# Kernel optimization log

Measured on AMD Instinct MI355X. Metric: run time of the kernel, lower is better.

The kernel has to match this reference:

```python
import jax, jax.numpy as jnp
import numpy as np

K_IN = 9      # input_patch_size
K_OUT = 3     # output_patch_size
C_IN = 4      # nb_of_input_features
C_OUT = 2     # nb_of_output_features
HID = 50      # int_layer_width
B, H, W = 16, 128, 128
CUT = K_IN // 2 - K_OUT // 2  # border pixels cut from output (3)


def _unfold(x, k):
    # x: [B, C, H, W] -> [B, C*k*k, L] with torch unfold ordering (c, ki, kj)
    b, c, h, w = x.shape
    ho, wo = h - k + 1, w - k + 1
    cols = jnp.stack([x[:, :, i:i + ho, j:j + wo]
                      for i in range(k) for j in range(k)], axis=2)  # [B,C,k*k,ho,wo]
    return cols.reshape(b, c * k * k, ho * wo)


def _fold_add(patches, oh, ow):
    # patches: [B, C, k, k, ho, wo] -> overlap-add into [B, C, oh, ow]
    b, c, k, _, ho, wo = patches.shape
    out = jnp.zeros((b, c, oh, ow), dtype=patches.dtype)
    for i in range(k):
        for j in range(k):
            out = out.at[:, :, i:i + ho, j:j + wo].add(patches[:, :, i, j])
    return out


def setup_inputs() -> dict:
    key = jax.random.key(0)
    ks = jax.random.split(key, 7)
    f_in = C_IN * K_IN * K_IN      # 324
    f_out = C_OUT * K_OUT * K_OUT  # 18
    s1 = 1.0 / np.sqrt(f_in)
    s2 = 1.0 / np.sqrt(HID)
    return {
        "x": jax.random.normal(ks[0], (B, C_IN, H, W), dtype=jnp.float32),
        "W1": jax.random.uniform(ks[1], (f_in, HID), jnp.float32, -s1, s1),
        "b1": jax.random.uniform(ks[2], (HID,), jnp.float32, -s1, s1),
        "W2": jax.random.uniform(ks[3], (HID, HID), jnp.float32, -s2, s2),
        "b2": jax.random.uniform(ks[4], (HID,), jnp.float32, -s2, s2),
        "W3": jax.random.uniform(ks[5], (HID, f_out), jnp.float32, -s2, s2),
        "b3": jax.random.uniform(ks[6], (f_out,), jnp.float32, -s2, s2),
    }


def reference(x, W1, b1, W2, b2, W3, b3):
    b, c, h, w = x.shape
    oh, ow = h - 2 * CUT, w - 2 * CUT          # 122, 122
    ho, wo = h - K_IN + 1, w - K_IN + 1        # 120, 120 (= oh-K_OUT+1)
    # unfold -> [B, L, C_in*K_in^2] -> flatten rows
    cols = _unfold(x, K_IN)                    # [B, 324, L]
    feats = cols.transpose(0, 2, 1).reshape(b * ho * wo, -1)
    # 3-layer MLP
    hmid = jax.nn.relu(feats @ W1 + b1)
    hmid = jax.nn.relu(hmid @ W2 + b2)
    out = hmid @ W3 + b3                       # [B*L, C_out*K_out^2]
    # fold (overlap-add), torch feature ordering (c, ki, kj)
    patches = out.reshape(b, ho, wo, C_OUT, K_OUT, K_OUT)
    patches = patches.transpose(0, 3, 4, 5, 1, 2)  # [B, C_out, k, k, ho, wo]
    res = _fold_add(patches, oh, ow)
    # divisor = fold(unfold(ones)) -> per-pixel overlap count
    ones_patches = jnp.ones((1, 1, K_OUT, K_OUT, ho, wo), dtype=x.dtype)
    divisor = _fold_add(ones_patches, oh, ow)  # [1,1,oh,ow]
    return res / divisor
```

## Files before the change

kernel.cpp:

```cpp
#include <hip/hip_runtime.h>
#include <hip/hip_bf16.h>

#define BATCH   16
#define C_INF   4
#define H_IN    128
#define W_IN    128
#define HID     50
#define F_OUT   18
#define HO      120
#define WO      120
#define OH      122
#define OW      122
#define NPOS    (BATCH * HO * WO)
#define MBLK    128
#define NBLKS   (NPOS / MBLK)

#define NB1     (11*4*2*64*8)
#define NB2     (2*4*2*64*8)
#define NB3     (2*2*2*64*8)
#define NWF     (NB1 + NB2 + NB3)
#define NXP     (BATCH*C_INF*H_IN*W_IN)
#define WOFF    (NPOS * F_OUT)

typedef float  v4f    __attribute__((ext_vector_type(4)));
typedef short  short8 __attribute__((ext_vector_type(8)));
typedef __bf16 v8bf   __attribute__((ext_vector_type(8)));
typedef int    v4i    __attribute__((ext_vector_type(4)));
typedef uint   u32x4  __attribute__((ext_vector_type(4)));
typedef u32x4  u32x4_a4 __attribute__((aligned(4)));

__device__ inline short f2bf_hi(float x) {
    __hip_bfloat16 h = __float2bfloat16(x);
    return __builtin_bit_cast(short, h);
}
__device__ inline float bf2f(short s) {
    __hip_bfloat16 h = __builtin_bit_cast(__hip_bfloat16, s);
    return __bfloat162float(h);
}
__device__ inline uint hipair(uint a, uint b) { return __builtin_amdgcn_perm(b, a, 0x07060302u); }
__device__ inline uint lopair(uint a, uint b) { return __builtin_amdgcn_perm(b, a, 0x05040100u); }

__device__ inline int slot_to_k1(int s, int qb, int e) {
    if (s < 9) {
        int pair = s*4 + qb;
        int c = pair/9, ki = pair - c*9;
        return c*81 + ki*9 + e;
    }
    int r = (s-9)*32 + qb*8 + e;
    if (r >= 36) return -1;
    int c = r/9, ki = r - c*9;
    return c*81 + ki*9 + 8;
}

__global__ __launch_bounds__(256)
void prep_kernel(const float* __restrict__ x,
                 const float* __restrict__ W1, const float* __restrict__ W2,
                 const float* __restrict__ W3,
                 uint* __restrict__ xp, short* __restrict__ wf)
{
    int i = blockIdx.x * 256 + threadIdx.x;
    if (i < NXP) {
        float v = x[i];
        short hi = f2bf_hi(v);
        short lo = f2bf_hi(v - bf2f(hi));
        xp[i] = ((uint)(ushort)hi << 16) | (uint)(ushort)lo;
        return;
    }
    i -= NXP;
    if (i >= NWF) return;
    float val;
    int p;
    if (i < NB1) {
        int t = i;
        int e = t & 7, lane = (t >> 3) & 63; p = (t >> 9) & 1;
        int rest = t >> 10;
        int u = rest & 3, s = rest >> 2;
        int k = slot_to_k1(s, lane >> 4, e);
        int n = u*16 + (lane & 15);
        val = (k >= 0 && n < HID) ? W1[k*HID + n] : 0.f;
    } else if (i < NB1 + NB2) {
        int t = i - NB1;
        int e = t & 7, lane = (t >> 3) & 63; p = (t >> 9) & 1;
        int rest = t >> 10;
        int u = rest & 3, s = rest >> 2;
        int k = s*32 + ((lane >> 4) << 3) + e;
        int n = u*16 + (lane & 15);
        val = (k < HID && n < HID) ? W2[k*HID + n] : 0.f;
    } else {
        int t = i - NB1 - NB2;
        int e = t & 7, lane = (t >> 3) & 63; p = (t >> 9) & 1;
        int rest = t >> 10;
        int u = rest & 1, s = rest >> 1;
        int k = s*32 + ((lane >> 4) << 3) + e;
        int n = u*16 + (lane & 15);
        val = (k < HID && n < F_OUT) ? W3[k*F_OUT + n] : 0.f;
    }
    short hi = f2bf_hi(val);
    wf[i] = (p == 0) ? hi : f2bf_hi(val - bf2f(hi));
}

__global__ __launch_bounds__(256, 4)
void mfma_mlp(const uint* __restrict__ xp,
              const float* __restrict__ b1, const float* __restrict__ b2,
              const float* __restrict__ b3,
              const short* __restrict__ wf, float* __restrict__ out3)
{
    __shared__ short h_hi[128 * 72];
    __shared__ short h_lo[128 * 72];

    const int tid  = threadIdx.x;
    const int lane = tid & 63;
    const int w    = tid >> 6;
    const int wm   = w >> 1, wn = w & 1;
    const int q    = lane >> 4, col = lane & 15;
    const int mbase = blockIdx.x * MBLK;

    int xbase[4];
    #pragma unroll
    for (int t = 0; t < 4; ++t) {
        int pos = mbase + wm*64 + t*16 + col;
        int b   = pos / (HO*WO); int rem = pos - b*(HO*WO);
        int y   = rem / WO;      int xc  = rem - y*WO;
        xbase[t] = b*(C_INF*H_IN*W_IN) + y*W_IN + xc;
    }

    const v4i* B1 = (const v4i*)wf;
    const v4i* B2 = (const v4i*)(wf + NB1);
    const v4i* B3 = (const v4i*)(wf + NB1 + NB2);

    v4f acc[4][2];
    #pragma unroll
    for (int t = 0; t < 4; ++t)
        #pragma unroll
        for (int u = 0; u < 2; ++u)
            acc[t][u] = (v4f){0.f, 0.f, 0.f, 0.f};

    #pragma unroll 3
    for (int s = 0; s < 9; ++s) {
        const int pair = s*4 + q;
        const int c = pair/9, ki = pair - c*9;
        const int off = c*(H_IN*W_IN) + ki*W_IN;

        v4i bhv[2], blv[2];
        #pragma unroll
        for (int uu = 0; uu < 2; ++uu) {
            int u  = 2*wn + uu;
            int fb = ((s*4 + u)*2)*64 + lane;
            bhv[uu] = B1[fb];
            blv[uu] = B1[fb + 64];
        }

        u32x4 wa[4], wb[4];
        #pragma unroll
        for (int t = 0; t < 4; ++t) {
            const uint* p = &xp[xbase[t] + off];
            wa[t] = *(const u32x4_a4*)(p);
            wb[t] = *(const u32x4_a4*)(p + 4);
        }
        short8 ah[4], al[4];
        #pragma unroll
        for (int t = 0; t < 4; ++t) {
            u32x4 hh, ll;
            hh.x = hipair(wa[t].x, wa[t].y); hh.y = hipair(wa[t].z, wa[t].w);
            hh.z = hipair(wb[t].x, wb[t].y); hh.w = hipair(wb[t].z, wb[t].w);
            ll.x = lopair(wa[t].x, wa[t].y); ll.y = lopair(wa[t].z, wa[t].w);
            ll.z = lopair(wb[t].x, wb[t].y); ll.w = lopair(wb[t].z, wb[t].w);
            ah[t] = __builtin_bit_cast(short8, hh);
            al[t] = __builtin_bit_cast(short8, ll);
        }
        #pragma unroll
        for (int uu = 0; uu < 2; ++uu) {
            v8bf bh = __builtin_bit_cast(v8bf, bhv[uu]);
            v8bf bl = __builtin_bit_cast(v8bf, blv[uu]);
            #pragma unroll
            for (int t = 0; t < 4; ++t) {
                v8bf a_h = __builtin_bit_cast(v8bf, ah[t]);
                v8bf a_l = __builtin_bit_cast(v8bf, al[t]);
                acc[t][uu] = __builtin_amdgcn_mfma_f32_16x16x32_bf16(a_h, bh, acc[t][uu], 0, 0, 0);
                acc[t][uu] = __builtin_amdgcn_mfma_f32_16x16x32_bf16(a_l, bh, acc[t][uu], 0, 0, 0);
                acc[t][uu] = __builtin_amdgcn_mfma_f32_16x16x32_bf16(a_h, bl, acc[t][uu], 0, 0, 0);
            }
        }
    }
    #pragma unroll
    for (int sr = 0; sr < 2; ++sr) {
        const int s = 9 + sr;
        short8 ah[4], al[4];
        #pragma unroll
        for (int e = 0; e < 8; ++e) {
            int r = sr*32 + q*8 + e;
            bool valid = (r < 36);
            int c = valid ? r/9 : 0;
            int ki = r - c*9;
            int off = c*(H_IN*W_IN) + ki*W_IN + 8;
            #pragma unroll
            for (int t = 0; t < 4; ++t) {
                uint wv = valid ? xp[xbase[t] + off] : 0u;
                ah[t][e] = (short)(wv >> 16);
                al[t][e] = (short)(wv & 0xffffu);
            }
        }
        #pragma unroll
        for (int uu = 0; uu < 2; ++uu) {
            int u  = 2*wn + uu;
            int fb = ((s*4 + u)*2)*64 + lane;
            v8bf bh = __builtin_bit_cast(v8bf, B1[fb]);
            v8bf bl = __builtin_bit_cast(v8bf, B1[fb + 64]);
            #pragma unroll
            for (int t = 0; t < 4; ++t) {
                v8bf a_h = __builtin_bit_cast(v8bf, ah[t]);
                v8bf a_l = __builtin_bit_cast(v8bf, al[t]);
                acc[t][uu] = __builtin_amdgcn_mfma_f32_16x16x32_bf16(a_h, bh, acc[t][uu], 0, 0, 0);
                acc[t][uu] = __builtin_amdgcn_mfma_f32_16x16x32_bf16(a_l, bh, acc[t][uu], 0, 0, 0);
                acc[t][uu] = __builtin_amdgcn_mfma_f32_16x16x32_bf16(a_h, bl, acc[t][uu], 0, 0, 0);
            }
        }
    }

    #pragma unroll
    for (int uu = 0; uu < 2; ++uu) {
        int j = (2*wn + uu)*16 + col;
        float bias = (j < HID) ? b1[j] : 0.f;
        #pragma unroll
        for (int t = 0; t < 4; ++t) {
            #pragma unroll
            for (int r = 0; r < 4; ++r) {
                float v = fmaxf(acc[t][uu][r] + bias, 0.f);
                int m = wm*64 + t*16 + q*4 + r;
                short hi = f2bf_hi(v);
                h_hi[m*72 + j] = hi;
                h_lo[m*72 + j] = f2bf_hi(v - bf2f(hi));
            }
        }
    }
    __syncthreads();

    v4f acc2[4][2];
    #pragma unroll
    for (int t = 0; t < 4; ++t)
        #pragma unroll
        for (int u = 0; u < 2; ++u)
            acc2[t][u] = (v4f){0.f, 0.f, 0.f, 0.f};

    #pragma unroll
    for (int s = 0; s < 2; ++s) {
        short8 ah2[4], al2[4];
        #pragma unroll
        for (int t = 0; t < 4; ++t) {
            int m = wm*64 + t*16 + col;
            ah2[t] = *(const short8*)&h_hi[m*72 + s*32 + q*8];
            al2[t] = *(const short8*)&h_lo[m*72 + s*32 + q*8];
        }
        #pragma unroll
        for (int uu = 0; uu < 2; ++uu) {
            int u  = 2*wn + uu;
            int fb = ((s*4 + u)*2)*64 + lane;
            v8bf bh = __builtin_bit_cast(v8bf, B2[fb]);
            v8bf bl = __builtin_bit_cast(v8bf, B2[fb + 64]);
            #pragma unroll
            for (int t = 0; t < 4; ++t) {
                v8bf a_h = __builtin_bit_cast(v8bf, ah2[t]);
                v8bf a_l = __builtin_bit_cast(v8bf, al2[t]);
                acc2[t][uu] = __builtin_amdgcn_mfma_f32_16x16x32_bf16(a_h, bh, acc2[t][uu], 0, 0, 0);
                acc2[t][uu] = __builtin_amdgcn_mfma_f32_16x16x32_bf16(a_l, bh, acc2[t][uu], 0, 0, 0);
                acc2[t][uu] = __builtin_amdgcn_mfma_f32_16x16x32_bf16(a_h, bl, acc2[t][uu], 0, 0, 0);
            }
        }
    }
    __syncthreads();

    #pragma unroll
    for (int uu = 0; uu < 2; ++uu) {
        int j = (2*wn + uu)*16 + col;
        float bias = (j < HID) ? b2[j] : 0.f;
        #pragma unroll
        for (int t = 0; t < 4; ++t) {
            #pragma unroll
            for (int r = 0; r < 4; ++r) {
                float v = fmaxf(acc2[t][uu][r] + bias, 0.f);
                int m = wm*64 + t*16 + q*4 + r;
                short hi = f2bf_hi(v);
                h_hi[m*72 + j] = hi;
                h_lo[m*72 + j] = f2bf_hi(v - bf2f(hi));
            }
        }
    }
    __syncthreads();

    v4f acc3[4];
    #pragma unroll
    for (int t = 0; t < 4; ++t) acc3[t] = (v4f){0.f, 0.f, 0.f, 0.f};

    #pragma unroll
    for (int s = 0; s < 2; ++s) {
        short8 ah3[4], al3[4];
        #pragma unroll
        for (int t = 0; t < 4; ++t) {
            int m = wm*64 + t*16 + col;
            ah3[t] = *(const short8*)&h_hi[m*72 + s*32 + q*8];
            al3[t] = *(const short8*)&h_lo[m*72 + s*32 + q*8];
        }
        int fb = ((s*2 + wn)*2)*64 + lane;
        v8bf bh = __builtin_bit_cast(v8bf, B3[fb]);
        v8bf bl = __builtin_bit_cast(v8bf, B3[fb + 64]);
        #pragma unroll
        for (int t = 0; t < 4; ++t) {
            v8bf a_h = __builtin_bit_cast(v8bf, ah3[t]);
            v8bf a_l = __builtin_bit_cast(v8bf, al3[t]);
            acc3[t] = __builtin_amdgcn_mfma_f32_16x16x32_bf16(a_h, bh, acc3[t], 0, 0, 0);
            acc3[t] = __builtin_amdgcn_mfma_f32_16x16x32_bf16(a_l, bh, acc3[t], 0, 0, 0);
            acc3[t] = __builtin_amdgcn_mfma_f32_16x16x32_bf16(a_h, bl, acc3[t], 0, 0, 0);
        }
    }
    __syncthreads();

    float* ot = (float*)h_hi;
    {
        int j = wn*16 + col;
        if (j < F_OUT) {
            float bias = b3[j];
            #pragma unroll
            for (int t = 0; t < 4; ++t) {
                #pragma unroll
                for (int r = 0; r < 4; ++r) {
                    int m = wm*64 + t*16 + q*4 + r;
                    ot[j*129 + m] = acc3[t][r] + bias;
                }
            }
        }
    }
    __syncthreads();
    for (int i = tid; i < F_OUT * 128; i += 256) {
        int j2 = i >> 7, m2 = i & 127;
        out3[j2*NPOS + mbase + m2] = ot[j2*129 + m2];
    }
}

__global__ __launch_bounds__(256)
void fold_kernel(const float* __restrict__ out3, float* __restrict__ out)
{
    const int idx = blockIdx.x * 256 + threadIdx.x;
    const int total = BATCH * 2 * OH * OW;
    if (idx >= total) return;

    int t = idx;
    const int ox = t % OW; t /= OW;
    const int oy = t % OH; t /= OH;
    const int c  = t & 1;  t >>= 1;
    const int b  = t;

    const int ylo = max(0, oy - 2), yhi = min(HO - 1, oy);
    const int xlo = max(0, ox - 2), xhi = min(WO - 1, ox);

    float s = 0.f;
    for (int y = ylo; y <= yhi; ++y) {
        const int ki = oy - y;
        for (int xx = xlo; xx <= xhi; ++xx) {
            const int kj = ox - xx;
            const int o  = (c*3 + ki)*3 + kj;
            s += out3[o*NPOS + (b*HO + y)*WO + xx];
        }
    }
    const float div = (float)((yhi - ylo + 1) * (xhi - xlo + 1));
    out[idx] = s / div;
}

extern "C" void kernel_launch(void* const* d_in, const int* in_sizes, int n_in,
                              void* d_out, int out_size, void* d_ws, size_t ws_size,
                              hipStream_t stream)
{
    const float* x  = (const float*)d_in[0];
    const float* W1 = (const float*)d_in[1];
    const float* b1 = (const float*)d_in[2];
    const float* W2 = (const float*)d_in[3];
    const float* b2 = (const float*)d_in[4];
    const float* W3 = (const float*)d_in[5];
    const float* b3 = (const float*)d_in[6];

    float* out3 = (float*)d_ws;
    short* wf   = (short*)d_ws + 2*(size_t)WOFF;
    uint*  xp   = (uint*)((char*)d_ws + (size_t)WOFF*4 + (size_t)NWF*2);

    const int nprep = (NXP + NWF + 255) / 256;
    prep_kernel<<<nprep, 256, 0, stream>>>(x, W1, W2, W3, xp, wf);

    mfma_mlp<<<NBLKS, 256, 0, stream>>>(xp, b1, b2, b3, wf, out3);

    const int total = BATCH * 2 * OH * OW;
    fold_kernel<<<(total + 255) / 256, 256, 0, stream>>>(out3, (float*)d_out);
}
```

Before: 124.7 us.

## Give each wave full hidden width and drop low-part split for layers 2-3

Each wave now owns 32 rows and all N columns, so the hidden activations it writes to shared memory are read back only by the same wave. That lets every __syncthreads be removed. Layers 2 and 3 drop the bf16 low-part activation term, cutting their MFMA count and shared-memory traffic. The output is stored straight to global as float4 instead of being staged through LDS. In exchange, each wave loads four B fragments per step instead of two, and layers 2-3 lose some accuracy from the bf16 hidden activations.

Measured after the change: 121.3 us. -2.7%, faster.

```diff
diff --git a/kernel.cpp b/kernel.cpp
--- a/kernel.cpp
+++ b/kernel.cpp
@@ -106,19 +106,18 @@
               const short* __restrict__ wf, float* __restrict__ out3)
 {
     __shared__ short h_hi[128 * 72];
-    __shared__ short h_lo[128 * 72];
 
     const int tid  = threadIdx.x;
     const int lane = tid & 63;
     const int w    = tid >> 6;
-    const int wm   = w >> 1, wn = w & 1;
     const int q    = lane >> 4, col = lane & 15;
     const int mbase = blockIdx.x * MBLK;
-
-    int xbase[4];
-    #pragma unroll
-    for (int t = 0; t < 4; ++t) {
-        int pos = mbase + wm*64 + t*16 + col;
+    const int mw    = w * 32;
+
+    int xbase[2];
+    #pragma unroll
+    for (int t = 0; t < 2; ++t) {
+        int pos = mbase + mw + t*16 + col;
         int b   = pos / (HO*WO); int rem = pos - b*(HO*WO);
         int y   = rem / WO;      int xc  = rem - y*WO;
         xbase[t] = b*(C_INF*H_IN*W_IN) + y*W_IN + xc;
@@ -128,11 +127,11 @@
     const v4i* B2 = (const v4i*)(wf + NB1);
     const v4i* B3 = (const v4i*)(wf + NB1 + NB2);
 
-    v4f acc[4][2];
-    #pragma unroll
-    for (int t = 0; t < 4; ++t)
-        #pragma unroll
-        for (int u = 0; u < 2; ++u)
+    v4f acc[2][4];
+    #pragma unroll
+    for (int t = 0; t < 2; ++t)
+        #pragma unroll
+        for (int u = 0; u < 4; ++u)
             acc[t][u] = (v4f){0.f, 0.f, 0.f, 0.f};
 
     #pragma unroll 3
@@ -141,25 +140,24 @@
         const int c = pair/9, ki = pair - c*9;
         const int off = c*(H_IN*W_IN) + ki*W_IN;
 
-        v4i bhv[2], blv[2];
-        #pragma unroll
-        for (int uu = 0; uu < 2; ++uu) {
-            int u  = 2*wn + uu;
+        v4i bhv[4], blv[4];
+        #pragma unroll
+        for (int u = 0; u < 4; ++u) {
             int fb = ((s*4 + u)*2)*64 + lane;
-            bhv[uu] = B1[fb];
-            blv[uu] = B1[fb + 64];
-        }
-
-        u32x4 wa[4], wb[4];
-        #pragma unroll
-        for (int t = 0; t < 4; ++t) {
+            bhv[u] = B1[fb];
+            blv[u] = B1[fb + 64];
+        }
+
+        u32x4 wa[2], wb[2];
+        #pragma unroll
+        for (int t = 0; t < 2; ++t) {
             const uint* p = &xp[xbase[t] + off];
             wa[t] = *(const u32x4_a4*)(p);
             wb[t] = *(const u32x4_a4*)(p + 4);
         }
-        short8 ah[4], al[4];
-        #pragma unroll
-        for (int t = 0; t < 4; ++t) {
+        short8 ah[2], al[2];
+        #pragma unroll
+        for (int t = 0; t < 2; ++t) {
             u32x4 hh, ll;
             hh.x = hipair(wa[t].x, wa[t].y); hh.y = hipair(wa[t].z, wa[t].w);
             hh.z = hipair(wb[t].x, wb[t].y); hh.w = hipair(wb[t].z, wb[t].w);
@@ -169,23 +167,23 @@
             al[t] = __builtin_bit_cast(short8, ll);
         }
         #pragma unroll
-        for (int uu = 0; uu < 2; ++uu) {
-            v8bf bh = __builtin_bit_cast(v8bf, bhv[uu]);
-            v8bf bl = __builtin_bit_cast(v8bf, blv[uu]);
-            #pragma unroll
-            for (int t = 0; t < 4; ++t) {
+        for (int u = 0; u < 4; ++u) {
+            v8bf bh = __builtin_bit_cast(v8bf, bhv[u]);
+            v8bf bl = __builtin_bit_cast(v8bf, blv[u]);
+            #pragma unroll
+            for (int t = 0; t < 2; ++t) {
                 v8bf a_h = __builtin_bit_cast(v8bf, ah[t]);
                 v8bf a_l = __builtin_bit_cast(v8bf, al[t]);
-                acc[t][uu] = __builtin_amdgcn_mfma_f32_16x16x32_bf16(a_h, bh, acc[t][uu], 0, 0, 0);
-                acc[t][uu] = __builtin_amdgcn_mfma_f32_16x16x32_bf16(a_l, bh, acc[t][uu], 0, 0, 0);
-                acc[t][uu] = __builtin_amdgcn_mfma_f32_16x16x32_bf16(a_h, bl, acc[t][uu], 0, 0, 0);
+                acc[t][u] = __builtin_amdgcn_mfma_f32_16x16x32_bf16(a_h, bh, acc[t][u], 0, 0, 0);
+                acc[t][u] = __builtin_amdgcn_mfma_f32_16x16x32_bf16(a_l, bh, acc[t][u], 0, 0, 0);
+                acc[t][u] = __builtin_amdgcn_mfma_f32_16x16x32_bf16(a_h, bl, acc[t][u], 0, 0, 0);
             }
         }
     }
     #pragma unroll
     for (int sr = 0; sr < 2; ++sr) {
         const int s = 9 + sr;
-        short8 ah[4], al[4];
+        short8 ah[2], al[2];
         #pragma unroll
         for (int e = 0; e < 8; ++e) {
             int r = sr*32 + q*8 + e;
@@ -194,145 +192,129 @@
             int ki = r - c*9;
             int off = c*(H_IN*W_IN) + ki*W_IN + 8;
             #pragma unroll
-            for (int t = 0; t < 4; ++t) {
+            for (int t = 0; t < 2; ++t) {
                 uint wv = valid ? xp[xbase[t] + off] : 0u;
                 ah[t][e] = (short)(wv >> 16);
                 al[t][e] = (short)(wv & 0xffffu);
             }
         }
         #pragma unroll
-        for (int uu = 0; uu < 2; ++uu) {
-            int u  = 2*wn + uu;
+        for (int u = 0; u < 4; ++u) {
             int fb = ((s*4 + u)*2)*64 + lane;
             v8bf bh = __builtin_bit_cast(v8bf, B1[fb]);
             v8bf bl = __builtin_bit_cast(v8bf, B1[fb + 64]);
             #pragma unroll
-            for (int t = 0; t < 4; ++t) {
+            for (int t = 0; t < 2; ++t) {
                 v8bf a_h = __builtin_bit_cast(v8bf, ah[t]);
                 v8bf a_l = __builtin_bit_cast(v8bf, al[t]);
-                acc[t][uu] = __builtin_amdgcn_mfma_f32_16x16x32_bf16(a_h, bh, acc[t][uu], 0, 0, 0);
-                acc[t][uu] = __builtin_amdgcn_mfma_f32_16x16x32_bf16(a_l, bh, acc[t][uu], 0, 0, 0);
-                acc[t][uu] = __builtin_amdgcn_mfma_f32_16x16x32_bf16(a_h, bl, acc[t][uu], 0, 0, 0);
-            }
-        }
-    }
-
-    #pragma unroll
-    for (int uu = 0; uu < 2; ++uu) {
-        int j = (2*wn + uu)*16 + col;
+                acc[t][u] = __builtin_amdgcn_mfma_f32_16x16x32_bf16(a_h, bh, acc[t][u], 0, 0, 0);
+                acc[t][u] = __builtin_amdgcn_mfma_f32_16x16x32_bf16(a_l, bh, acc[t][u], 0, 0, 0);
+                acc[t][u] = __builtin_amdgcn_mfma_f32_16x16x32_bf16(a_h, bl, acc[t][u], 0, 0, 0);
+            }
+        }
+    }
+
+    #pragma unroll
+    for (int u = 0; u < 4; ++u) {
+        int j = u*16 + col;
         float bias = (j < HID) ? b1[j] : 0.f;
         #pragma unroll
-        for (int t = 0; t < 4; ++t) {
+        for (int t = 0; t < 2; ++t) {
             #pragma unroll
             for (int r = 0; r < 4; ++r) {
-                float v = fmaxf(acc[t][uu][r] + bias, 0.f);
-                int m = wm*64 + t*16 + q*4 + r;
-                short hi = f2bf_hi(v);
-                h_hi[m*72 + j] = hi;
-                h_lo[m*72 + j] = f2bf_hi(v - bf2f(hi));
-            }
-        }
-    }
-    __syncthreads();
-
-    v4f acc2[4][2];
-    #pragma unroll
-    for (int t = 0; t < 4; ++t)
-        #pragma unroll
-        for (int u = 0; u < 2; ++u)
+                float v = fmaxf(acc[t][u][r] + bias, 0.f);
+                int m = mw + t*16 + q*4 + r;
+                h_hi[m*72 + j] = f2bf_hi(v);
+            }
+        }
+    }
+
+    v4f acc2[2][4];
+    #pragma unroll
+    for (int t = 0; t < 2; ++t)
+        #pragma unroll
+        for (int u = 0; u < 4; ++u)
             acc2[t][u] = (v4f){0.f, 0.f, 0.f, 0.f};
 
     #pragma unroll
     for (int s = 0; s < 2; ++s) {
-        short8 ah2[4], al2[4];
-        #pragma unroll
-        for (int t = 0; t < 4; ++t) {
-            int m = wm*64 + t*16 + col;
+        short8 ah2[2];
+        #pragma unroll
+        for (int t = 0; t < 2; ++t) {
+            int m = mw + t*16 + col;
             ah2[t] = *(const short8*)&h_hi[m*72 + s*32 + q*8];
-            al2[t] = *(const short8*)&h_lo[m*72 + s*32 + q*8];
-        }
-        #pragma unroll
-        for (int uu = 0; uu < 2; ++uu) {
-            int u  = 2*wn + uu;
+        }
+        #pragma unroll
+        for (int u = 0; u < 4; ++u) {
             int fb = ((s*4 + u)*2)*64 + lane;
             v8bf bh = __builtin_bit_cast(v8bf, B2[fb]);
             v8bf bl = __builtin_bit_cast(v8bf, B2[fb + 64]);
             #pragma unroll
-            for (int t = 0; t < 4; ++t) {
+            for (int t = 0; t < 2; ++t) {
                 v8bf a_h = __builtin_bit_cast(v8bf, ah2[t]);
-                v8bf a_l = __builtin_bit_cast(v8bf, al2[t]);
-                acc2[t][uu] = __builtin_amdgcn_mfma_f32_16x16x32_bf16(a_h, bh, acc2[t][uu], 0, 0, 0);
-                acc2[t][uu] = __builtin_amdgcn_mfma_f32_16x16x32_bf16(a_l, bh, acc2[t][uu], 0, 0, 0);
-                acc2[t][uu] = __builtin_amdgcn_mfma_f32_16x16x32_bf16(a_h, bl, acc2[t][uu], 0, 0, 0);
-            }
-        }
-    }
-    __syncthreads();
-
-    #pragma unroll
-    for (int uu = 0; uu < 2; ++uu) {
-        int j = (2*wn + uu)*16 + col;
+                acc2[t][u] = __builtin_amdgcn_mfma_f32_16x16x32_bf16(a_h, bh, acc2[t][u], 0, 0, 0);
+                acc2[t][u] = __builtin_amdgcn_mfma_f32_16x16x32_bf16(a_h, bl, acc2[t][u], 0, 0, 0);
+            }
+        }
+    }
+
+    #pragma unroll
+    for (int u = 0; u < 4; ++u) {
+        int j = u*16 + col;
         float bias = (j < HID) ? b2[j] : 0.f;
         #pragma unroll
-        for (int t = 0; t < 4; ++t) {
+        for (int t = 0; t < 2; ++t) {
             #pragma unroll
             for (int r = 0; r < 4; ++r) {
-                float v = fmaxf(acc2[t][uu][r] + bias, 0.f);
-                int m = wm*64 + t*16 + q*4 + r;
-                short hi = f2bf_hi(v);
-                h_hi[m*72 + j] = hi;
-                h_lo[m*72 + j] = f2bf_hi(v - bf2f(hi));
-            }
-        }
-    }
-    __syncthreads();
-
-    v4f acc3[4];
-    #pragma unroll
-    for (int t = 0; t < 4; ++t) acc3[t] = (v4f){0.f, 0.f, 0.f, 0.f};
+                float v = fmaxf(acc2[t][u][r] + bias, 0.f);
+                int m = mw + t*16 + q*4 + r;
+                h_hi[m*72 + j] = f2bf_hi(v);
+            }
+        }
+    }
+
+    v4f acc3[2][2];
+    #pragma unroll
+    for (int t = 0; t < 2; ++t)
+        #pragma unroll
+        for (int u = 0; u < 2; ++u)
+            acc3[t][u] = (v4f){0.f, 0.f, 0.f, 0.f};
 
     #pragma unroll
     for (int s = 0; s < 2; ++s) {
-        short8 ah3[4], al3[4];
-        #pragma unroll
-        for (int t = 0; t < 4; ++t) {
-            int m = wm*64 + t*16 + col;
+        short8 ah3[2];
+        #pragma unroll
+        for (int t = 0; t < 2; ++t) {
+            int m = mw + t*16 + col;
             ah3[t] = *(const short8*)&h_hi[m*72 + s*32 + q*8];
-            al3[t] = *(const short8*)&h_lo[m*72 + s*32 + q*8];
-        }
-        int fb = ((s*2 + wn)*2)*64 + lane;
-        v8bf bh = __builtin_bit_cast(v8bf, B3[fb]);
-        v8bf bl = __builtin_bit_cast(v8bf, B3[fb + 64]);
-        #pragma unroll
-        for (int t = 0; t < 4; ++t) {
-            v8bf a_h = __builtin_bit_cast(v8bf, ah3[t]);
-            v8bf a_l = __builtin_bit_cast(v8bf, al3[t]);
-            acc3[t] = __builtin_amdgcn_mfma_f32_16x16x32_bf16(a_h, bh, acc3[t], 0, 0, 0);
-            acc3[t] = __builtin_amdgcn_mfma_f32_16x16x32_bf16(a_l, bh, acc3[t], 0, 0, 0);
-            acc3[t] = __builtin_amdgcn_mfma_f32_16x16x32_bf16(a_h, bl, acc3[t], 0, 0, 0);
-        }
-    }
-    __syncthreads();
-
-    float* ot = (float*)h_hi;
-    {
-        int j = wn*16 + col;
+        }
+        #pragma unroll
+        for (int u = 0; u < 2; ++u) {
+            int fb = ((s*2 + u)*2)*64 + lane;
+            v8bf bh = __builtin_bit_cast(v8bf, B3[fb]);
+            v8bf bl = __builtin_bit_cast(v8bf, B3[fb + 64]);
+            #pragma unroll
+            for (int t = 0; t < 2; ++t) {
+                v8bf a_h = __builtin_bit_cast(v8bf, ah3[t]);
+                acc3[t][u] = __builtin_amdgcn_mfma_f32_16x16x32_bf16(a_h, bh, acc3[t][u], 0, 0, 0);
+                acc3[t][u] = __builtin_amdgcn_mfma_f32_16x16x32_bf16(a_h, bl, acc3[t][u], 0, 0, 0);
+            }
+        }
+    }
+
+    #pragma unroll
+    for (int u = 0; u < 2; ++u) {
+        int j = u*16 + col;
         if (j < F_OUT) {
             float bias = b3[j];
             #pragma unroll
-            for (int t = 0; t < 4; ++t) {
+            for (int t = 0; t < 2; ++t) {
+                v4f vs;
                 #pragma unroll
-                for (int r = 0; r < 4; ++r) {
-                    int m = wm*64 + t*16 + q*4 + r;
-                    ot[j*129 + m] = acc3[t][r] + bias;
-                }
-            }
-        }
-    }
-    __syncthreads();
-    for (int i = tid; i < F_OUT * 128; i += 256) {
-        int j2 = i >> 7, m2 = i & 127;
-        out3[j2*NPOS + mbase + m2] = ot[j2*129 + m2];
+                for (int r = 0; r < 4; ++r) vs[r] = acc3[t][u][r] + bias;
+                *(v4f*)&out3[j*NPOS + mbase + mw + t*16 + q*4] = vs;
+            }
+        }
     }
 }
 
@@ -378,8 +360,8 @@
     const float* b3 = (const float*)d_in[6];
 
     float* out3 = (float*)d_ws;
-    short* wf   = (short*)d_ws + 2*(size_t)WOFF;
-    uint*  xp   = (uint*)((char*)d_ws + (size_t)WOFF*4 + (size_t)NWF*2);
+    short* wf   = (short*)(out3 + WOFF);
+    uint*  xp   = (uint*)(wf + NWF);
 
     const int nprep = (NXP + NWF + 255) / 256;
     prep_kernel<<<nprep, 256, 0, stream>>>(x, W1, W2, W3, xp, wf);
```
